# Kernel optimization log

Measured on AMD Instinct MI355X. Metric: run time of the kernel, lower is better.

## Reference

```python
import jax, jax.numpy as jnp
import numpy as np

B, T, C_EMBD, C_ATT = 16, 1024, 2048, 2048


def wkv(time_decay, time_first, k, v):
    """Numerically-stable RWKV WKV recurrence (matches wkv_cuda).
    time_decay/time_first: [C]; k, v: [B, T, C] -> y: [B, T, C]."""
    w = -jnp.exp(time_decay)  # [C], decay is -exp(param)
    u = time_first
    Bn, Tn, Cn = k.shape

    def step(carry, kv_t):
        aa, bb, pp = carry          # each [B, C]
        kt, vt = kv_t               # [B, C]
        ww = u + kt
        p = jnp.maximum(pp, ww)
        e1 = jnp.exp(pp - p)
        e2 = jnp.exp(ww - p)
        y = (e1 * aa + e2 * vt) / (e1 * bb + e2)
        ww2 = pp + w
        p2 = jnp.maximum(ww2, kt)
        e1b = jnp.exp(ww2 - p2)
        e2b = jnp.exp(kt - p2)
        new = (e1b * aa + e2b * vt, e1b * bb + e2b, p2)
        return new, y

    init = (jnp.zeros((Bn, Cn), k.dtype),
            jnp.zeros((Bn, Cn), k.dtype),
            jnp.full((Bn, Cn), -1e38, k.dtype))
    kT = jnp.swapaxes(k, 0, 1)  # [T, B, C]
    vT = jnp.swapaxes(v, 0, 1)
    _, ys = jax.lax.scan(step, init, (kT, vT))
    return jnp.swapaxes(ys, 0, 1)  # [B, T, C]


def setup_inputs() -> dict:
    key = jax.random.key(0)
    ks = jax.random.split(key, 10)
    xav = np.sqrt(2.0 / (C_EMBD + C_ATT))
    inp = {
        "x": jax.random.normal(ks[0], (B, T, C_EMBD), jnp.float32),
        "time_decay": jax.random.normal(ks[1], (C_ATT,), jnp.float32) * 0.02,
        "time_first": jax.random.normal(ks[2], (C_ATT,), jnp.float32) * 0.02,
        "time_mix_k": jax.random.normal(ks[3], (1, 1, C_EMBD), jnp.float32) * 0.02,
        "time_mix_v": jax.random.normal(ks[4], (1, 1, C_EMBD), jnp.float32) * 0.02,
        "time_mix_r": jax.random.normal(ks[5], (1, 1, C_EMBD), jnp.float32) * 0.02,
        "key_w": jax.random.normal(ks[6], (C_ATT, C_EMBD), jnp.float32) * xav,
        "value_w": jax.random.normal(ks[7], (C_ATT, C_EMBD), jnp.float32) * xav,
        "receptance_w": jax.random.normal(ks[8], (C_ATT, C_EMBD), jnp.float32) * xav,
        "output_w": jax.random.normal(ks[9], (C_EMBD, C_ATT), jnp.float32) * xav,
    }
    return inp


def reference(x, time_decay, time_first, time_mix_k, time_mix_v, time_mix_r,
              key_w, value_w, receptance_w, output_w):
    # time shift: xx[:, t] = x[:, t-1], xx[:, 0] = 0
    xx = jnp.pad(x, ((0, 0), (1, 0), (0, 0)))[:, :-1]
    xk = x * time_mix_k + xx * (1 - time_mix_k)
    xv = x * time_mix_v + xx * (1 - time_mix_v)
    xr = x * time_mix_r + xx * (1 - time_mix_r)
    k = jnp.einsum('btc,dc->btd', xk, key_w)
    v = jnp.einsum('btc,dc->btd', xv, value_w)
    r = jnp.einsum('btc,dc->btd', xr, receptance_w)
    sr = jax.nn.sigmoid(r)
    rwkv = sr * wkv(time_decay, time_first, k, v)
    return jnp.einsum('btd,cd->btc', rwkv, output_w)
```

## Files before the change

### kernel.cpp

```cpp
#include <hip/hip_runtime.h>
#include <hip/hip_bf16.h>

#define BB 16
#define TT 1024
#define CC 2048
#define TS 32

typedef __attribute__((ext_vector_type(4))) float f32x4;
typedef __attribute__((ext_vector_type(8))) short bf16x8;

__device__ __forceinline__ unsigned short f2bf(float f) {
  union { float f; unsigned u; } x; x.f = f;
  unsigned r = x.u + 0x7fffu + ((x.u >> 16) & 1u);
  return (unsigned short)(r >> 16);
}
__device__ __forceinline__ float bf2f(unsigned short u) {
  union { unsigned u; float f; } x; x.u = ((unsigned)u) << 16;
  return x.f;
}

__device__ __forceinline__ ushort4 mix4(float4 a, float4 b, float4 m) {
  ushort4 o;
  o.x = f2bf(a.x * m.x + b.x * (1.f - m.x));
  o.y = f2bf(a.y * m.y + b.y * (1.f - m.y));
  o.z = f2bf(a.z * m.z + b.z * (1.f - m.z));
  o.w = f2bf(a.w * m.w + b.w * (1.f - m.w));
  return o;
}

__global__ void f2bf_all(const float* __restrict__ w0, const float* __restrict__ w1,
                         const float* __restrict__ w2, const float* __restrict__ w3,
                         unsigned short* __restrict__ o0, unsigned short* __restrict__ o1,
                         unsigned short* __restrict__ o2, unsigned short* __restrict__ o3,
                         int n4each) {
  const float* ws[4] = {w0, w1, w2, w3};
  unsigned short* os[4] = {o0, o1, o2, o3};
  int total = 4 * n4each;
  for (int i = blockIdx.x * blockDim.x + threadIdx.x; i < total;
       i += gridDim.x * blockDim.x) {
    int seg = i / n4each, j = i - seg * n4each;
    float4 v = ((const float4*)ws[seg])[j];
    ushort4 o;
    o.x = f2bf(v.x); o.y = f2bf(v.y); o.z = f2bf(v.z); o.w = f2bf(v.w);
    ((ushort4*)os[seg])[j] = o;
  }
}

__global__ void mix_kernel(const float* __restrict__ x,
                           const float* __restrict__ tmk,
                           const float* __restrict__ tmv,
                           const float* __restrict__ tmr,
                           unsigned short* __restrict__ xk,
                           unsigned short* __restrict__ xv,
                           unsigned short* __restrict__ xr,
                           int t0, int Tc) {
  const int C4 = CC / 4;
  const int total = BB * Tc * C4;
  for (int g = blockIdx.x * blockDim.x + threadIdx.x; g < total;
       g += gridDim.x * blockDim.x) {
    int cg = g % C4;
    int lrow = g / C4;
    int tl = lrow % Tc;
    int b = lrow / Tc;
    int t = t0 + tl;
    size_t gidx = (size_t)(b * TT + t) * C4 + cg;
    float4 xc = ((const float4*)x)[gidx];
    float4 xp = make_float4(0.f, 0.f, 0.f, 0.f);
    if (t > 0) xp = ((const float4*)x)[gidx - C4];
    ((ushort4*)xk)[g] = mix4(xc, xp, ((const float4*)tmk)[cg]);
    ((ushort4*)xv)[g] = mix4(xc, xp, ((const float4*)tmv)[cg]);
    ((ushort4*)xr)[g] = mix4(xc, xp, ((const float4*)tmr)[cg]);
  }
}

template<bool BF16OUT>
__global__ __launch_bounds__(512, 2)
void gemm256(const unsigned short* __restrict__ A,
             const unsigned short* __restrict__ B,
             void* __restrict__ Cv, int N, int K, int tcShift, int t0) {
  __shared__ __align__(1024) unsigned char lds[131072];
  const int tid = threadIdx.x;
  const int lane = tid & 63;
  const int wid = tid >> 6;
  const int wr = wid >> 2;
  const int wc = wid & 3;

  const int nwg = gridDim.x;
  const int cpx = nwg >> 3;
  const int bid = blockIdx.x;
  const int wg = (bid & 7) * cpx + (bid >> 3);
  const int bcolN = N >> 8;
  const int brow = wg / bcolN;
  const int bcol = wg % bcolN;

  const int strow = tid >> 2;
  const int scelem = (((tid & 3) ^ ((tid >> 3) & 3)) << 3);
  const unsigned short* sA0 = A + (size_t)(brow * 256 + strow) * K + scelem;
  const unsigned short* sA1 = A + (size_t)(brow * 256 + 128 + strow) * K + scelem;
  const unsigned short* sB0 = B + (size_t)(bcol * 256 + strow) * K + scelem;
  const unsigned short* sB1 = B + (size_t)(bcol * 256 + 128 + strow) * K + scelem;

  const int frow = lane & 15;
  const int fhi = (lane >> 4) << 4;
  const int fsw = ((frow >> 1) & 3) << 4;
  const int aOff = (wr * 128 + frow) * 64 + (fhi ^ fsw);
  const int bOff = 65536 + (wc * 64 + frow) * 64 + (fhi ^ fsw);
  const int ldsW = wid * 1024;

#define STG(ptr, ldsOff, eoff)                                                 \
  __builtin_amdgcn_global_load_lds(                                            \
      (const __attribute__((address_space(1))) void*)((ptr) + (eoff)),         \
      (__attribute__((address_space(3))) void*)(lds + (ldsOff) + ldsW),        \
      16, 0, 0)
#define STAGE_TILE(BUF, eoff) do {                                             \
    STG(sA0, (BUF) * 16384, eoff);                                             \
    STG(sA1, (BUF) * 16384 + 8192, eoff);                                      \
    STG(sB0, 65536 + (BUF) * 16384, eoff);                                     \
    STG(sB1, 65536 + (BUF) * 16384 + 8192, eoff);                              \
  } while (0)

#define RDT(BUF) do {                                                          \
    _Pragma("unroll") for (int am = 0; am < 8; ++am)                           \
      af[am] = *(const bf16x8*)(lds + aOff + (BUF) * 16384 + am * 1024);       \
    _Pragma("unroll") for (int an = 0; an < 4; ++an)                           \
      bf[an] = *(const bf16x8*)(lds + bOff + (BUF) * 16384 + an * 1024);       \
  } while (0)

#define MFMAT do {                                                             \
    __builtin_amdgcn_s_setprio(1);                                             \
    _Pragma("unroll") for (int am = 0; am < 8; ++am)                           \
    _Pragma("unroll") for (int an = 0; an < 4; ++an)                           \
      acc[am][an] = __builtin_amdgcn_mfma_f32_16x16x32_bf16(                   \
          af[am], bf[an], acc[am][an], 0, 0, 0);                               \
    __builtin_amdgcn_s_setprio(0);                                             \
  } while (0)

#define SB __builtin_amdgcn_sched_barrier(0)
#define BAR __builtin_amdgcn_s_barrier()

  f32x4 acc[8][4] = {};
  bf16x8 af[8], bf[4];

  STAGE_TILE(0, 0);
  STAGE_TILE(1, 32);
  STAGE_TILE(2, 64);
  SB;
  asm volatile("s_waitcnt vmcnt(8)" ::: "memory");
  BAR;

  for (int g = 0; g < 15; ++g) {
#define TILE_BODY(J)                                                           \
    RDT(J);                                                                    \
    STAGE_TILE((J + 3) & 3, (3 + J) * 32);                                     \
    SB;                                                                        \
    asm volatile("s_waitcnt vmcnt(8)" ::: "memory");                           \
    BAR;                                                                       \
    MFMAT;
    TILE_BODY(0)
    TILE_BODY(1)
    TILE_BODY(2)
    TILE_BODY(3)
#undef TILE_BODY
    sA0 += 128; sA1 += 128; sB0 += 128; sB1 += 128;
  }

  RDT(0);
  STAGE_TILE(3, 96);
  SB;
  asm volatile("s_waitcnt vmcnt(8)" ::: "memory");
  BAR;
  MFMAT;

  RDT(1);
  SB;
  asm volatile("s_waitcnt vmcnt(4)" ::: "memory");
  BAR;
  MFMAT;

  RDT(2);
  SB;
  asm volatile("s_waitcnt vmcnt(0)" ::: "memory");
  BAR;
  MFMAT;

  RDT(3);
  MFMAT;

#undef STG
#undef STAGE_TILE
#undef RDT
#undef MFMAT
#undef SB
#undef BAR

  const int crow0 = (lane >> 4) << 2;
  const int ccol = lane & 15;
  const int tcMask = (1 << tcShift) - 1;
#pragma unroll
  for (int am = 0; am < 8; ++am)
#pragma unroll
    for (int an = 0; an < 4; ++an) {
      const int col = bcol * 256 + wc * 64 + an * 16 + ccol;
#pragma unroll
      for (int j = 0; j < 4; ++j) {
        int r = brow * 256 + wr * 128 + am * 16 + crow0 + j;
        int orow = ((r >> tcShift) << 10) + t0 + (r & tcMask);
        if (BF16OUT)
          ((unsigned short*)Cv)[(size_t)orow * N + col] = f2bf(acc[am][an][j]);
        else
          ((float*)Cv)[(size_t)orow * N + col] = acc[am][an][j];
      }
    }
}

__global__ void wkv_part(const float* __restrict__ time_decay,
                         const unsigned short* __restrict__ k,
                         const unsigned short* __restrict__ v,
                         float* __restrict__ paA, float* __restrict__ paB,
                         float* __restrict__ paP, int Tc) {
  int idx = blockIdx.x * blockDim.x + threadIdx.x;
  int c = idx & (CC - 1);
  int b = (idx >> 11) & (BB - 1);
  int s = idx >> 15;
  float w = -__expf(time_decay[c]);
  float aa = 0.f, bb = 0.f, pp = -1e38f;
  size_t base = ((size_t)b * Tc + s * TS) * CC + c;
  for (int t = 0; t < TS; ++t) {
    size_t off = base + (size_t)t * CC;
    float kt = bf2f(k[off]), vt = bf2f(v[off]);
    float ww2 = pp + w;
    float p2 = fmaxf(ww2, kt);
    float e1 = __expf(ww2 - p2), e2 = __expf(kt - p2);
    aa = e1 * aa + e2 * vt;
    bb = e1 * bb + e2;
    pp = p2;
  }
  paA[idx] = aa; paB[idx] = bb; paP[idx] = pp;
}

__global__ void wkv_comb(const float* __restrict__ time_decay,
                         const float* __restrict__ paA,
                         const float* __restrict__ paB,
                         const float* __restrict__ paP,
                         float* __restrict__ inA, float* __restrict__ inB,
                         float* __restrict__ inP,
                         float* __restrict__ state, int S, int t0) {
  int idx = blockIdx.x * blockDim.x + threadIdx.x;
  int c = idx & (CC - 1);
  float w = -__expf(time_decay[c]);
  float wTs = w * (float)TS;
  float A, Bv, P;
  if (t0 == 0) { A = 0.f; Bv = 0.f; P = -1e38f; }
  else { A = state[idx]; Bv = state[32768 + idx]; P = state[65536 + idx]; }
  for (int s = 0; s < S; ++s) {
    size_t o = (size_t)s * 32768 + idx;
    inA[o] = A; inB[o] = Bv; inP[o] = P;
    float Pd = P + wTs;
    float Ps = paP[o];
    float Pn = fmaxf(Pd, Ps);
    float e1 = __expf(Pd - Pn), e2 = __expf(Ps - Pn);
    A = e1 * A + e2 * paA[o];
    Bv = e1 * Bv + e2 * paB[o];
    P = Pn;
  }
  state[idx] = A; state[32768 + idx] = Bv; state[65536 + idx] = P;
}

__global__ void wkv_out(const float* __restrict__ time_decay,
                        const float* __restrict__ time_first,
                        const unsigned short* __restrict__ k,
                        const unsigned short* __restrict__ v,
                        const unsigned short* __restrict__ r,
                        unsigned short* __restrict__ rwkv,
                        const float* __restrict__ inA,
                        const float* __restrict__ inB,
                        const float* __restrict__ inP, int Tc) {
  int idx = blockIdx.x * blockDim.x + threadIdx.x;
  int c = idx & (CC - 1);
  int b = (idx >> 11) & (BB - 1);
  int s = idx >> 15;
  float w = -__expf(time_decay[c]);
  float u = time_first[c];
  float aa = inA[idx], bb = inB[idx], pp = inP[idx];
  size_t base = ((size_t)b * Tc + s * TS) * CC + c;
  for (int t = 0; t < TS; ++t) {
    size_t off = base + (size_t)t * CC;
    float kt = bf2f(k[off]), vt = bf2f(v[off]);
    float ww = u + kt;
    float p = fmaxf(pp, ww);
    float e1 = __expf(pp - p), e2 = __expf(ww - p);
    float y = (e1 * aa + e2 * vt) / (e1 * bb + e2);
    float rr = bf2f(r[off]);
    float sr = 1.f / (1.f + __expf(-rr));
    rwkv[off] = f2bf(sr * y);
    float ww2 = pp + w;
    float p2 = fmaxf(ww2, kt);
    float e1b = __expf(ww2 - p2), e2b = __expf(kt - p2);
    aa = e1b * aa + e2b * vt;
    bb = e1b * bb + e2b;
    pp = p2;
  }
}

extern "C" void kernel_launch(void* const* d_in, const int* in_sizes, int n_in,
                              void* d_out, int out_size, void* d_ws,
                              size_t ws_size, hipStream_t stream) {
  const float* x          = (const float*)d_in[0];
  const float* time_decay = (const float*)d_in[1];
  const float* time_first = (const float*)d_in[2];
  const float* tmk        = (const float*)d_in[3];
  const float* tmv        = (const float*)d_in[4];
  const float* tmr        = (const float*)d_in[5];
  const float* key_w      = (const float*)d_in[6];
  const float* value_w    = (const float*)d_in[7];
  const float* rec_w      = (const float*)d_in[8];
  const float* out_w      = (const float*)d_in[9];
  float* out = (float*)d_out;

  const size_t WW = (size_t)CC * CC;
  const size_t wtBytes = 4 * WW * 2;
  const size_t stBytes = 3 * (size_t)BB * CC * 4;

  int Tc = 1024;
  while (Tc > 32) {
    size_t chunkBytes = (size_t)BB * Tc * CC * 12;
    if (wtBytes + stBytes + chunkBytes + 1024 <= ws_size) break;
    Tc >>= 1;
  }
  const int Mc = BB * Tc;
  const size_t NC = (size_t)Mc * CC;
  const int S = Tc / TS;

  char* p = (char*)d_ws;
  unsigned short* wk  = (unsigned short*)p; p += WW * 2;
  unsigned short* wv  = (unsigned short*)p; p += WW * 2;
  unsigned short* wrr = (unsigned short*)p; p += WW * 2;
  unsigned short* wo  = (unsigned short*)p; p += WW * 2;
  float* state        = (float*)p;          p += stBytes;
  unsigned short* kbuf= (unsigned short*)p; p += NC * 2;
  unsigned short* vbuf= (unsigned short*)p; p += NC * 2;
  unsigned short* xk  = (unsigned short*)p; p += NC * 2;
  unsigned short* xv  = (unsigned short*)p; p += NC * 2;
  unsigned short* xr  = (unsigned short*)p; p += NC * 2;
  unsigned short* rbuf= (unsigned short*)p; p += NC * 2;
  unsigned short* rwkv = xk;

  const size_t SBt = (size_t)S * 32768;
  float* paA = (float*)xv;
  float* paB = paA + SBt;
  float* paP = paB + SBt;
  float* inA = paP + SBt;
  float* inB = inA + SBt;
  float* inP = inB + SBt;

  f2bf_all<<<2048, 256, 0, stream>>>(key_w, value_w, rec_w, out_w,
                                     wk, wv, wrr, wo, (int)(WW / 4));

  int tcShift = 0;
  while ((1 << tcShift) < Tc) ++tcShift;

  const int nwg = (Mc / 256) * (CC / 256);
  int mixBlocks = (Mc * (CC / 4) + 255) / 256;
  if (mixBlocks > 4096) mixBlocks = 4096;

  for (int t0 = 0; t0 < TT; t0 += Tc) {
    mix_kernel<<<mixBlocks, 256, 0, stream>>>(x, tmk, tmv, tmr, xk, xv, xr,
                                              t0, Tc);
    gemm256<true><<<nwg, 512, 0, stream>>>(xk, wk, kbuf, CC, CC, 10, 0);
    gemm256<true><<<nwg, 512, 0, stream>>>(xv, wv, vbuf, CC, CC, 10, 0);
    wkv_part<<<S * 128, 256, 0, stream>>>(time_decay, kbuf, vbuf,
                                          paA, paB, paP, Tc);
    gemm256<true><<<nwg, 512, 0, stream>>>(xr, wrr, rbuf, CC, CC, 10, 0);
    wkv_comb<<<128, 256, 0, stream>>>(time_decay, paA, paB, paP,
                                      inA, inB, inP, state, S, t0);
    wkv_out<<<S * 128, 256, 0, stream>>>(time_decay, time_first, kbuf, vbuf,
                                         rbuf, rwkv, inA, inB, inP, Tc);
    gemm256<false><<<nwg, 512, 0, stream>>>(rwkv, wo, out, CC, CC,
                                            tcShift, t0);
  }
}
```

Before: 738.5 us.

## Double-buffer LDS fragment registers to overlap LDS reads with MFMA

Splits the A/B fragment registers into two sets so that reads of the next k-tile from LDS are issued while MFMAs run on the current tile's fragments. The vmcnt waits are tightened so a tile is resident one step earlier, and the barrier now comes after the MFMAs instead of between the LDS read and the MFMA. The aim is to hide LDS read latency behind matrix math. In exchange it roughly doubles fragment register use, which could lower occupancy or cause spills, and the barrier ordering needs care to avoid overwriting a buffer that another wave is still reading.

```diff
diff --git a/kernel.cpp b/kernel.cpp
--- a/kernel.cpp
+++ b/kernel.cpp
@@ -119,72 +119,63 @@
     STG(sB1, 65536 + (BUF) * 16384 + 8192, eoff);                              \
   } while (0)
 
-#define RDT(BUF) do {                                                          \
+#define RDT(BUF, AF, BF) do {                                                  \
     _Pragma("unroll") for (int am = 0; am < 8; ++am)                           \
-      af[am] = *(const bf16x8*)(lds + aOff + (BUF) * 16384 + am * 1024);       \
+      AF[am] = *(const bf16x8*)(lds + aOff + (BUF) * 16384 + am * 1024);       \
     _Pragma("unroll") for (int an = 0; an < 4; ++an)                           \
-      bf[an] = *(const bf16x8*)(lds + bOff + (BUF) * 16384 + an * 1024);       \
+      BF[an] = *(const bf16x8*)(lds + bOff + (BUF) * 16384 + an * 1024);       \
   } while (0)
 
-#define MFMAT do {                                                             \
+#define MFMAT(AF, BF) do {                                                     \
     __builtin_amdgcn_s_setprio(1);                                             \
     _Pragma("unroll") for (int am = 0; am < 8; ++am)                           \
     _Pragma("unroll") for (int an = 0; an < 4; ++an)                           \
       acc[am][an] = __builtin_amdgcn_mfma_f32_16x16x32_bf16(                   \
-          af[am], bf[an], acc[am][an], 0, 0, 0);                               \
+          AF[am], BF[an], acc[am][an], 0, 0, 0);                               \
     __builtin_amdgcn_s_setprio(0);                                             \
   } while (0)
 
 #define SB __builtin_amdgcn_sched_barrier(0)
 #define BAR __builtin_amdgcn_s_barrier()
+#define VMC(n) asm volatile("s_waitcnt vmcnt(" #n ")" ::: "memory")
 
   f32x4 acc[8][4] = {};
-  bf16x8 af[8], bf[4];
+  bf16x8 afA[8], bfA[4], afB[8], bfB[4];
 
   STAGE_TILE(0, 0);
   STAGE_TILE(1, 32);
   STAGE_TILE(2, 64);
   SB;
-  asm volatile("s_waitcnt vmcnt(8)" ::: "memory");
+  VMC(4);
   BAR;
+  RDT(0, afA, bfA);
 
   for (int g = 0; g < 15; ++g) {
-#define TILE_BODY(J)                                                           \
-    RDT(J);                                                                    \
+#define TILE_BODY(J, CURA, CURB, NXTA, NXTB)                                   \
     STAGE_TILE((J + 3) & 3, (3 + J) * 32);                                     \
+    RDT((J + 1) & 3, NXTA, NXTB);                                              \
+    MFMAT(CURA, CURB);                                                         \
     SB;                                                                        \
-    asm volatile("s_waitcnt vmcnt(8)" ::: "memory");                           \
-    BAR;                                                                       \
-    MFMAT;
-    TILE_BODY(0)
-    TILE_BODY(1)
-    TILE_BODY(2)
-    TILE_BODY(3)
+    VMC(4);                                                                    \
+    BAR;
+    TILE_BODY(0, afA, bfA, afB, bfB)
+    TILE_BODY(1, afB, bfB, afA, bfA)
+    TILE_BODY(2, afA, bfA, afB, bfB)
+    TILE_BODY(3, afB, bfB, afA, bfA)
 #undef TILE_BODY
     sA0 += 128; sA1 += 128; sB0 += 128; sB1 += 128;
   }
 
-  RDT(0);
   STAGE_TILE(3, 96);
-  SB;
-  asm volatile("s_waitcnt vmcnt(8)" ::: "memory");
-  BAR;
-  MFMAT;
-
-  RDT(1);
-  SB;
-  asm volatile("s_waitcnt vmcnt(4)" ::: "memory");
-  BAR;
-  MFMAT;
-
-  RDT(2);
-  SB;
-  asm volatile("s_waitcnt vmcnt(0)" ::: "memory");
-  BAR;
-  MFMAT;
-
-  RDT(3);
-  MFMAT;
+  RDT(1, afB, bfB);
+  MFMAT(afA, bfA);
+  SB; VMC(4); BAR;
+  RDT(2, afA, bfA);
+  MFMAT(afB, bfB);
+  SB; VMC(0); BAR;
+  RDT(3, afB, bfB);
+  MFMAT(afA, bfA);
+  MFMAT(afB, bfB);
 
 #undef STG
 #undef STAGE_TILE
@@ -192,6 +183,7 @@
 #undef MFMAT
 #undef SB
 #undef BAR
+#undef VMC
 
   const int crow0 = (lane >> 4) << 2;
   const int ccol = lane & 15;
```

New measurement: 1.117 ms. 51.3% more time.

## Stagger LDS reads across wave groups and shorten GEMM prefetch depth

Applied to the files above, without the earlier changes.

The GEMM main loop now prefetches two tiles ahead instead of three, and splits the 8 waves into two groups. Group A reads its LDS fragments before the barrier and group B after it, so LDS reads and MFMA phases of the two groups overlap in a ping-pong pattern. This aims to reduce LDS bank contention and keep the matrix units busier. The shallower prefetch leaves less time to hide global-memory latency, and the extra scheduling barriers limit compiler reordering.

```diff
diff --git a/kernel.cpp b/kernel.cpp
--- a/kernel.cpp
+++ b/kernel.cpp
@@ -84,6 +84,7 @@
   const int wid = tid >> 6;
   const int wr = wid >> 2;
   const int wc = wid & 3;
+  const bool grpA = (wid < 4);
 
   const int nwg = gridDim.x;
   const int cpx = nwg >> 3;
@@ -137,24 +138,27 @@
 
 #define SB __builtin_amdgcn_sched_barrier(0)
 #define BAR __builtin_amdgcn_s_barrier()
+#define VMC(n) asm volatile("s_waitcnt vmcnt(" #n ")" ::: "memory")
 
   f32x4 acc[8][4] = {};
   bf16x8 af[8], bf[4];
 
   STAGE_TILE(0, 0);
   STAGE_TILE(1, 32);
-  STAGE_TILE(2, 64);
   SB;
-  asm volatile("s_waitcnt vmcnt(8)" ::: "memory");
+  VMC(4);
   BAR;
+  SB;
 
   for (int g = 0; g < 15; ++g) {
 #define TILE_BODY(J)                                                           \
-    RDT(J);                                                                    \
-    STAGE_TILE((J + 3) & 3, (3 + J) * 32);                                     \
+    STAGE_TILE((J + 2) & 3, (2 + J) * 32);                                     \
+    if (grpA) RDT(J & 3);                                                      \
     SB;                                                                        \
-    asm volatile("s_waitcnt vmcnt(8)" ::: "memory");                           \
+    VMC(4);                                                                    \
     BAR;                                                                       \
+    SB;                                                                        \
+    if (!grpA) RDT(J & 3);                                                     \
     MFMAT;
     TILE_BODY(0)
     TILE_BODY(1)
@@ -164,25 +168,20 @@
     sA0 += 128; sA1 += 128; sB0 += 128; sB1 += 128;
   }
 
-  RDT(0);
+  STAGE_TILE(2, 64);
+  if (grpA) RDT(0);
+  SB; VMC(4); BAR; SB;
+  if (!grpA) RDT(0);
+  MFMAT;
   STAGE_TILE(3, 96);
-  SB;
-  asm volatile("s_waitcnt vmcnt(8)" ::: "memory");
-  BAR;
+  if (grpA) RDT(1);
+  SB; VMC(4); BAR; SB;
+  if (!grpA) RDT(1);
   MFMAT;
-
-  RDT(1);
-  SB;
-  asm volatile("s_waitcnt vmcnt(4)" ::: "memory");
-  BAR;
+  if (grpA) RDT(2);
+  SB; VMC(0); BAR; SB;
+  if (!grpA) RDT(2);
   MFMAT;
-
-  RDT(2);
-  SB;
-  asm volatile("s_waitcnt vmcnt(0)" ::: "memory");
-  BAR;
-  MFMAT;
-
   RDT(3);
   MFMAT;
 
@@ -192,6 +191,7 @@
 #undef MFMAT
 #undef SB
 #undef BAR
+#undef VMC
 
   const int crow0 = (lane >> 4) << 2;
   const int ccol = lane & 15;
```

New measurement: 738.6 us. No clear change (+0.0%).
